# Optimization experiments

Measured on AMD Instinct MI355X. Metric: run time of the kernel, lower is better.

## Reference

```python
import jax, jax.numpy as jnp
import numpy as np

EMBED_DIM = 1024
NUM_HEADS = 16
HEAD_DIM = EMBED_DIM // NUM_HEADS
SCALING = HEAD_DIM ** -0.5
W_SCALE = 0.02  # small init so exp(scores) in focused path stays finite


def setup_inputs() -> dict:
    key = jax.random.key(0)
    ks = jax.random.split(key, 12)
    B, T = 2, 2048
    hidden_states = jax.random.normal(ks[0], (B, T, EMBED_DIM), dtype=jnp.float32)
    focused_attention = jax.random.uniform(ks[1], (B, T, T), dtype=jnp.float32)
    def lin(kw, kb):
        W = jax.random.normal(kw, (EMBED_DIM, EMBED_DIM), dtype=jnp.float32) * W_SCALE
        b = jax.random.normal(kb, (EMBED_DIM,), dtype=jnp.float32) * W_SCALE
        return W, b
    Wq, bq = lin(ks[2], ks[3])
    Wk, bk = lin(ks[4], ks[5])
    Wv, bv = lin(ks[6], ks[7])
    Wo, bo = lin(ks[8], ks[9])
    return {"hidden_states": hidden_states, "focused_attention": focused_attention,
            "Wq": Wq, "bq": bq, "Wk": Wk, "bk": bk, "Wv": Wv, "bv": bv, "Wo": Wo, "bo": bo}


def reference(hidden_states, focused_attention, Wq, bq, Wk, bk, Wv, bv, Wo, bo):
    B, T, D = hidden_states.shape
    H, hd = NUM_HEADS, HEAD_DIM

    def shape_heads(x):  # [B,T,D] -> [B,H,T,hd]
        return x.reshape(B, T, H, hd).transpose(0, 2, 1, 3)

    q = shape_heads((hidden_states @ Wq.T + bq) * SCALING)
    k = shape_heads(hidden_states @ Wk.T + bk)
    v = shape_heads(hidden_states @ Wv.T + bv)

    # [B,H,T,S] raw attention logits
    scores = jnp.einsum('bhtd,bhsd->bhts', q, k)

    # focused_attention path: exp-weighted normalization (not a plain softmax)
    f = focused_attention[:, None, :, :]  # broadcast over heads
    e = f * jnp.exp(scores)
    attn = e / jnp.sum(e, axis=-1, keepdims=True)

    out = jnp.einsum('bhts,bhsd->bhtd', attn, v)  # [B,H,T,hd]
    out = out.transpose(0, 2, 1, 3).reshape(B, T, D)
    return out @ Wo.T + bo
```

## Files before the change

### kernel.cpp

```cpp
#include <hip/hip_runtime.h>
#include <stdint.h>


typedef __attribute__((ext_vector_type(8))) short short8;
typedef __attribute__((ext_vector_type(4))) short short4v;
typedef __attribute__((ext_vector_type(4))) float f32x4;
typedef unsigned short u16;

#define T_SEQ 2048
#define NH    16
#define HD    64
#define DM    1024

__device__ __forceinline__ float b2f(u16 h) {
  union { unsigned u; float f; } v; v.u = ((unsigned)h) << 16; return v.f;
}
__device__ __forceinline__ u16 f2bf(float x) {
  union { float f; unsigned u; } v; v.f = x;
  unsigned r = v.u + 0x7fffu + ((v.u >> 16) & 1u);
  return (u16)(r >> 16);
}
__device__ __forceinline__ short8 cvt8(const float* p) {
  const f32x4 a = *(const f32x4*)p;
  const f32x4 b = *(const f32x4*)(p + 4);
  short8 o;
  o[0] = (short)f2bf(a[0]); o[1] = (short)f2bf(a[1]);
  o[2] = (short)f2bf(a[2]); o[3] = (short)f2bf(a[3]);
  o[4] = (short)f2bf(b[0]); o[5] = (short)f2bf(b[1]);
  o[6] = (short)f2bf(b[2]); o[7] = (short)f2bf(b[3]);
  return o;
}
__device__ __forceinline__ void gl_lds16(const void* g, void* l) {
  __builtin_amdgcn_global_load_lds(
      (const __attribute__((address_space(1))) void*)g,
      (__attribute__((address_space(3))) void*)l, 16, 0, 0);
}

#define HS_CH 524288u
#define F_CH  1048576u
#define W_CH  131072u
__global__ void cvt_kernel(const float* __restrict__ hs, const float* __restrict__ f,
                           const float* __restrict__ Wq, const float* __restrict__ Wk,
                           const float* __restrict__ Wv, const float* __restrict__ Wo,
                           u16* __restrict__ hsb, u16* __restrict__ fb,
                           u16* __restrict__ Wqb, u16* __restrict__ Wkb,
                           u16* __restrict__ Wvb, u16* __restrict__ Wob) {
  unsigned c = blockIdx.x * 256 + threadIdx.x;
  const float* s; u16* d; unsigned off;
  if (c < HS_CH)                       { s = hs; d = hsb; off = c; }
  else if ((c -= HS_CH) < F_CH)        { s = f;  d = fb;  off = c; }
  else if ((c -= F_CH) < W_CH)         { s = Wq; d = Wqb; off = c; }
  else if ((c -= W_CH) < W_CH)         { s = Wk; d = Wkb; off = c; }
  else if ((c -= W_CH) < W_CH)         { s = Wv; d = Wvb; off = c; }
  else                                 { s = Wo; d = Wob; off = c - W_CH; }
  *(short8*)&d[(size_t)off * 8] = cvt8(&s[(size_t)off * 8]);
}

__global__ __launch_bounds__(256, 4) void qkv_kernel(
    const void* __restrict__ Xv,
    const void* __restrict__ Wqv, const float* __restrict__ bq,
    const void* __restrict__ Wkv, const float* __restrict__ bk,
    const void* __restrict__ Wvv, const float* __restrict__ bv,
    int isf32,
    u16* __restrict__ q, u16* __restrict__ k, u16* __restrict__ v)
{
  const int z = blockIdx.z;
  const void* Wp = (z == 0) ? Wqv : (z == 1) ? Wkv : Wvv;
  const float* bias = (z == 0) ? bq : (z == 1) ? bk : bv;

  __shared__ alignas(16) short lsA[4][128][8];
  __shared__ alignas(16) short lsB[4][128][8];

  const int tid = threadIdx.x;
  const int lane = tid & 63;
  const int wv = tid >> 6;
  const int lq = lane >> 4, li = lane & 15;
  const int wm = wv >> 1, wn = wv & 1;

  const int m0 = blockIdx.y * 128;
  const int n0 = blockIdx.x * 128;

  f32x4 acc[4][4];
#pragma unroll
  for (int i = 0; i < 4; i++)
#pragma unroll
    for (int j = 0; j < 4; j++) acc[i][j] = (f32x4){0.f, 0.f, 0.f, 0.f};

  for (int k0 = 0; k0 < DM; k0 += 32) {
    if (isf32) {
      const float* X32 = (const float*)Xv;
      const float* W32 = (const float*)Wp;
#pragma unroll
      for (int r = 0; r < 2; ++r) {
        const int idx = tid + 256 * r;
        const int row = idx >> 2, slab = idx & 3;
        *(short8*)&lsA[slab][row][0] = cvt8(&X32[(size_t)(m0 + row) * DM + k0 + slab * 8]);
        *(short8*)&lsB[slab][row][0] = cvt8(&W32[(size_t)(n0 + row) * DM + k0 + slab * 8]);
      }
    } else {
      const u16* X16 = (const u16*)Xv;
      const u16* W16 = (const u16*)Wp;
#pragma unroll
      for (int r = 0; r < 2; ++r) {
        const int row = r * 64 + lane;
        gl_lds16(&X16[(size_t)(m0 + row) * DM + k0 + wv * 8], &lsA[wv][row][0]);
        gl_lds16(&W16[(size_t)(n0 + row) * DM + k0 + wv * 8], &lsB[wv][row][0]);
      }
    }
    __syncthreads();
    short8 af[4], bf[4];
#pragma unroll
    for (int mt = 0; mt < 4; ++mt)
      af[mt] = *(const short8*)&lsA[lq][wm * 64 + mt * 16 + li][0];
#pragma unroll
    for (int nt = 0; nt < 4; ++nt)
      bf[nt] = *(const short8*)&lsB[lq][wn * 64 + nt * 16 + li][0];
#pragma unroll
    for (int mt = 0; mt < 4; ++mt)
#pragma unroll
      for (int nt = 0; nt < 4; ++nt)
        acc[mt][nt] = __builtin_amdgcn_mfma_f32_16x16x32_bf16(af[mt], bf[nt], acc[mt][nt], 0, 0, 0);
    __syncthreads();
  }

  float bs[4];
#pragma unroll
  for (int nt = 0; nt < 4; ++nt) bs[nt] = bias[n0 + wn * 64 + nt * 16 + li];
  const float scale = (z == 0) ? 0.125f : 1.0f;

  if (z != 2) {
    u16* dst = (z == 0) ? q : k;
#pragma unroll
    for (int mt = 0; mt < 4; ++mt) {
      const int mbase = m0 + wm * 64 + mt * 16 + lq * 4;
#pragma unroll
      for (int nt = 0; nt < 4; ++nt) {
        const int n = n0 + wn * 64 + nt * 16 + li;
        const int h = n >> 6, d = n & 63;
#pragma unroll
        for (int r = 0; r < 4; ++r) {
          const int m = mbase + r;
          const int b = m >> 11, t = m & (T_SEQ - 1);
          dst[((size_t)(b * NH + h) * T_SEQ + t) * HD + d] = f2bf((acc[mt][nt][r] + bs[nt]) * scale);
        }
      }
    }
  } else {
#pragma unroll
    for (int mt = 0; mt < 4; ++mt) {
      const int mbase = m0 + wm * 64 + mt * 16 + lq * 4;
      const int b = mbase >> 11, t = mbase & (T_SEQ - 1);
#pragma unroll
      for (int nt = 0; nt < 4; ++nt) {
        const int n = n0 + wn * 64 + nt * 16 + li;
        const int h = n >> 6, d = n & 63;
        u16 pk[4];
#pragma unroll
        for (int r = 0; r < 4; ++r) pk[r] = f2bf(acc[mt][nt][r] + bs[nt]);
        *(short4v*)&v[((size_t)(b * NH + h) * HD + d) * T_SEQ + t] = *(const short4v*)pk;
      }
    }
  }
}

__global__ __launch_bounds__(256, 2) void attn_kernel(
    const u16* __restrict__ q, const u16* __restrict__ k,
    const u16* __restrict__ v, const void* __restrict__ fv,
    int isf32, u16* __restrict__ ao)
{
  __shared__ alignas(16) u16 Kl[2][8192];
  __shared__ alignas(16) u16 Vl[2][8192];
  __shared__ alignas(16) u16 pPf[4][2048];

  const int tid = threadIdx.x;
  const int w = tid >> 6;
  const int lane = tid & 63;
  const int lq = lane >> 4, li = lane & 15;

  const int t0 = blockIdx.x * 128;
  const int h = blockIdx.y;
  const int b = blockIdx.z;

  const u16* qh = q + (size_t)(b * NH + h) * T_SEQ * HD;
  const u16* kh = k + (size_t)(b * NH + h) * T_SEQ * HD;
  const u16* vh = v + (size_t)(b * NH + h) * HD * T_SEQ;

  short8 qf[2][2];
#pragma unroll
  for (int g = 0; g < 2; ++g)
#pragma unroll
    for (int kk = 0; kk < 2; ++kk)
      qf[g][kk] = *(const short8*)&qh[(size_t)(t0 + w * 32 + g * 16 + li) * HD + kk * 32 + lq * 8];

  f32x4 oacc[2][4];
#pragma unroll
  for (int g = 0; g < 2; ++g)
#pragma unroll
    for (int j = 0; j < 4; j++) oacc[g][j] = (f32x4){0.f, 0.f, 0.f, 0.f};
  float den[2] = {0.f, 0.f};

#define STAGE_TILE(S0, BUF)                                                      \
  {                                                                              \
    const u16* gK = kh + (size_t)(S0) * HD;                                      \
    const u16* gV = vh + (S0);                                                   \
    u16* Kb = &Kl[BUF][0];                                                       \
    u16* Vb = &Vl[BUF][0];                                                       \
    _Pragma("unroll")                                                            \
    for (int r = 0; r < 4; ++r) {                                                \
      const int L = (w * 4 + r) * 64 + lane;                                     \
      const int sl = L >> 3, jx = L & 7, j = jx ^ (sl & 7);                      \
      gl_lds16(gK + (size_t)sl * HD + j * 8, Kb + (size_t)L * 8);                \
      const int d = L >> 4, scx = L & 15, sc = scx ^ (d & 15);                   \
      gl_lds16(gV + (size_t)d * T_SEQ + sc * 8, Vb + (size_t)L * 8);             \
    }                                                                            \
  }

  STAGE_TILE(0, 0)
  __syncthreads();

  for (int it = 0; it < 16; ++it) {
    const int cur = it & 1;
    const int s0 = it * 128;
    if (it < 15) STAGE_TILE(s0 + 128, cur ^ 1)

    const u16* Kb = &Kl[cur][0];
    const u16* Vb = &Vl[cur][0];

    short8 kf[2][8];
#pragma unroll
    for (int kk = 0; kk < 2; ++kk)
#pragma unroll
      for (int mt = 0; mt < 8; ++mt) {
        const int sl = mt * 16 + li;
        const int c = sl * 8 + ((kk * 4 + lq) ^ (sl & 7));
        kf[kk][mt] = *(const short8*)&Kb[(size_t)c * 8];
      }
    short8 vf[4][4];
#pragma unroll
    for (int kk = 0; kk < 4; ++kk)
#pragma unroll
      for (int dn = 0; dn < 4; ++dn) {
        const int d = dn * 16 + li;
        const int c = d * 16 + ((kk * 4 + lq) ^ (d & 15));
        vf[kk][dn] = *(const short8*)&Vb[(size_t)c * 8];
      }

    u16* pw = &pPf[w][0];
#pragma unroll
    for (int g = 0; g < 2; ++g) {
      f32x4 sacc[8];
#pragma unroll
      for (int mt = 0; mt < 8; ++mt) sacc[mt] = (f32x4){0.f, 0.f, 0.f, 0.f};
#pragma unroll
      for (int kk = 0; kk < 2; ++kk)
#pragma unroll
        for (int mt = 0; mt < 8; ++mt)
          sacc[mt] = __builtin_amdgcn_mfma_f32_16x16x32_bf16(kf[kk][mt], qf[g][kk], sacc[mt], 0, 0, 0);

      const int tg = t0 + w * 32 + g * 16 + li;
#pragma unroll
      for (int mt = 0; mt < 8; ++mt) {
        u16 pk[4];
        if (isf32) {
          const float* fb = (const float*)fv + (size_t)b * T_SEQ * T_SEQ;
          const f32x4 fr = *(const f32x4*)&fb[(size_t)tg * T_SEQ + s0 + mt * 16 + lq * 4];
#pragma unroll
          for (int r = 0; r < 4; ++r) {
            const float e = __expf(fminf(sacc[mt][r], 60.0f));
            const float p = fr[r] * e;
            den[g] += p;
            pk[r] = f2bf(p);
          }
        } else {
          const u16* fb = (const u16*)fv + (size_t)b * T_SEQ * T_SEQ;
          const short4v fr = *(const short4v*)&fb[(size_t)tg * T_SEQ + s0 + mt * 16 + lq * 4];
#pragma unroll
          for (int r = 0; r < 4; ++r) {
            const float e = __expf(fminf(sacc[mt][r], 60.0f));
            const float p = b2f((u16)fr[r]) * e;
            den[g] += p;
            pk[r] = f2bf(p);
          }
        }
        const int c8 = (mt * 4 + lq) ^ ((li & 7) << 1);
        *(short4v*)&pw[li * 128 + c8 * 4] = *(const short4v*)pk;
      }

#pragma unroll
      for (int kk = 0; kk < 4; ++kk) {
        const int c8 = ((kk << 3) + (lq << 1)) ^ ((li & 7) << 1);
        const short8 pf = *(const short8*)&pw[li * 128 + c8 * 4];
#pragma unroll
        for (int dn = 0; dn < 4; ++dn)
          oacc[g][dn] = __builtin_amdgcn_mfma_f32_16x16x32_bf16(pf, vf[kk][dn], oacc[g][dn], 0, 0, 0);
      }
    }
    __syncthreads();
  }

#pragma unroll
  for (int g = 0; g < 2; ++g) {
    den[g] += __shfl_xor(den[g], 16, 64);
    den[g] += __shfl_xor(den[g], 32, 64);
  }

#pragma unroll
  for (int g = 0; g < 2; ++g) {
#pragma unroll
    for (int r = 0; r < 4; ++r) {
      const float rd = 1.0f / __shfl(den[g], lq * 4 + r, 64);
      const int t = t0 + w * 32 + g * 16 + lq * 4 + r;
#pragma unroll
      for (int dn = 0; dn < 4; ++dn)
        ao[(size_t)(b * T_SEQ + t) * DM + h * HD + dn * 16 + li] = f2bf(oacc[g][dn][r] * rd);
    }
  }
#undef STAGE_TILE
}

__global__ __launch_bounds__(256, 4) void oproj_kernel(
    const u16* __restrict__ A, const void* __restrict__ Wov,
    const float* __restrict__ bo, int isf32, float* __restrict__ out)
{
  __shared__ alignas(16) short lsA[4][128][8];
  __shared__ alignas(16) short lsB[4][128][8];

  const int tid = threadIdx.x;
  const int lane = tid & 63;
  const int wv = tid >> 6;
  const int lq = lane >> 4, li = lane & 15;
  const int wm = wv >> 1, wn = wv & 1;

  const int m0 = blockIdx.y * 128;
  const int n0 = blockIdx.x * 128;

  f32x4 acc[4][4];
#pragma unroll
  for (int i = 0; i < 4; i++)
#pragma unroll
    for (int j = 0; j < 4; j++) acc[i][j] = (f32x4){0.f, 0.f, 0.f, 0.f};

  for (int k0 = 0; k0 < DM; k0 += 32) {
#pragma unroll
    for (int r = 0; r < 2; ++r) {
      const int row = r * 64 + lane;
      gl_lds16(&A[(size_t)(m0 + row) * DM + k0 + wv * 8], &lsA[wv][row][0]);
    }
    if (isf32) {
      const float* W32 = (const float*)Wov;
#pragma unroll
      for (int r = 0; r < 2; ++r) {
        const int idx = tid + 256 * r;
        const int row = idx >> 2, slab = idx & 3;
        *(short8*)&lsB[slab][row][0] = cvt8(&W32[(size_t)(n0 + row) * DM + k0 + slab * 8]);
      }
    } else {
      const u16* W16 = (const u16*)Wov;
#pragma unroll
      for (int r = 0; r < 2; ++r) {
        const int row = r * 64 + lane;
        gl_lds16(&W16[(size_t)(n0 + row) * DM + k0 + wv * 8], &lsB[wv][row][0]);
      }
    }
    __syncthreads();
    short8 af[4], bf[4];
#pragma unroll
    for (int mt = 0; mt < 4; ++mt)
      af[mt] = *(const short8*)&lsA[lq][wm * 64 + mt * 16 + li][0];
#pragma unroll
    for (int nt = 0; nt < 4; ++nt)
      bf[nt] = *(const short8*)&lsB[lq][wn * 64 + nt * 16 + li][0];
#pragma unroll
    for (int mt = 0; mt < 4; ++mt)
#pragma unroll
      for (int nt = 0; nt < 4; ++nt)
        acc[mt][nt] = __builtin_amdgcn_mfma_f32_16x16x32_bf16(af[mt], bf[nt], acc[mt][nt], 0, 0, 0);
    __syncthreads();
  }

  float bs[4];
#pragma unroll
  for (int nt = 0; nt < 4; ++nt) bs[nt] = bo[n0 + wn * 64 + nt * 16 + li];

#pragma unroll
  for (int mt = 0; mt < 4; ++mt) {
    const int mbase = m0 + wm * 64 + mt * 16 + lq * 4;
#pragma unroll
    for (int nt = 0; nt < 4; ++nt) {
      const int n = n0 + wn * 64 + nt * 16 + li;
#pragma unroll
      for (int r = 0; r < 4; ++r)
        out[(size_t)(mbase + r) * DM + n] = acc[mt][nt][r] + bs[nt];
    }
  }
}

extern "C" void kernel_launch(void* const* d_in, const int* in_sizes, int n_in,
                              void* d_out, int out_size, void* d_ws, size_t ws_size,
                              hipStream_t stream) {
  (void)in_sizes; (void)n_in; (void)out_size;
  const float* hs = (const float*)d_in[0];
  const float* fa = (const float*)d_in[1];
  const float* Wq = (const float*)d_in[2];
  const float* bq = (const float*)d_in[3];
  const float* Wk = (const float*)d_in[4];
  const float* bk = (const float*)d_in[5];
  const float* Wv = (const float*)d_in[6];
  const float* bv = (const float*)d_in[7];
  const float* Wo = (const float*)d_in[8];
  const float* bo = (const float*)d_in[9];
  float* out = (float*)d_out;

  const size_t NEED = 256 + 2u * (8388608u + 4194304u + 4u * 1048576u + 4u * 4194304u);
  char* base = (char*)d_ws + 256;
  if (ws_size >= NEED) {
    u16* fb  = (u16*)base;
    u16* hsb = fb + 8388608u;
    u16* Wqb = hsb + 4194304u;
    u16* Wkb = Wqb + 1048576u;
    u16* Wvb = Wkb + 1048576u;
    u16* Wob = Wvb + 1048576u;
    u16* qw  = Wob + 1048576u;
    u16* kw  = qw + 4194304u;
    u16* vw  = kw + 4194304u;
    u16* aw  = vw + 4194304u;
    cvt_kernel<<<8192, 256, 0, stream>>>(hs, fa, Wq, Wk, Wv, Wo, hsb, fb, Wqb, Wkb, Wvb, Wob);
    qkv_kernel<<<dim3(8, 32, 3), 256, 0, stream>>>(hsb, Wqb, bq, Wkb, bk, Wvb, bv, 0, qw, kw, vw);
    attn_kernel<<<dim3(16, 16, 2), 256, 0, stream>>>(qw, kw, vw, fb, 0, aw);
    oproj_kernel<<<dim3(8, 32, 1), 256, 0, stream>>>(aw, Wob, bo, 0, out);
  } else {
    u16* qw = (u16*)base;
    u16* kw = qw + 4194304u;
    u16* vw = kw + 4194304u;
    u16* aw = vw + 4194304u;
    qkv_kernel<<<dim3(8, 32, 3), 256, 0, stream>>>(hs, Wq, bq, Wk, bk, Wv, bv, 1, qw, kw, vw);
    attn_kernel<<<dim3(16, 16, 2), 256, 0, stream>>>(qw, kw, vw, fa, 1, aw);
    oproj_kernel<<<dim3(8, 32, 1), 256, 0, stream>>>(aw, Wo, bo, 1, out);
  }
}
```

Measured before the change: 341.8 us.

## Prefetch focused-attention tile into registers; store Q/K token-major; stage V transpose via LDS

The attention kernel now loads the next tile's focused_attention values into registers, converted to bf16, while the current tile computes. The loop is unrolled by two to ping-pong between the two register buffers, which hides global-load latency on the largest input stream. Q and K are written in plain [B,T,D] layout with coalesced stores, and the V transpose goes through shared memory so it can use wide 16-byte stores. The cost is more register pressure and the removal of the fminf clamp on the exponent. Rounding f to bf16 in the fp32 path may also change accuracy slightly.

```diff
diff --git a/kernel.cpp b/kernel.cpp
--- a/kernel.cpp
+++ b/kernel.cpp
@@ -68,8 +68,9 @@
   const void* Wp = (z == 0) ? Wqv : (z == 1) ? Wkv : Wvv;
   const float* bias = (z == 0) ? bq : (z == 1) ? bk : bv;
 
-  __shared__ alignas(16) short lsA[4][128][8];
-  __shared__ alignas(16) short lsB[4][128][8];
+  __shared__ alignas(16) u16 smem[17408];
+  u16* lsA = smem;
+  u16* lsB = smem + 4096;
 
   const int tid = threadIdx.x;
   const int lane = tid & 63;
@@ -94,8 +95,8 @@
       for (int r = 0; r < 2; ++r) {
         const int idx = tid + 256 * r;
         const int row = idx >> 2, slab = idx & 3;
-        *(short8*)&lsA[slab][row][0] = cvt8(&X32[(size_t)(m0 + row) * DM + k0 + slab * 8]);
-        *(short8*)&lsB[slab][row][0] = cvt8(&W32[(size_t)(n0 + row) * DM + k0 + slab * 8]);
+        *(short8*)&lsA[(slab * 128 + row) * 8] = cvt8(&X32[(size_t)(m0 + row) * DM + k0 + slab * 8]);
+        *(short8*)&lsB[(slab * 128 + row) * 8] = cvt8(&W32[(size_t)(n0 + row) * DM + k0 + slab * 8]);
       }
     } else {
       const u16* X16 = (const u16*)Xv;
@@ -103,18 +104,18 @@
 #pragma unroll
       for (int r = 0; r < 2; ++r) {
         const int row = r * 64 + lane;
-        gl_lds16(&X16[(size_t)(m0 + row) * DM + k0 + wv * 8], &lsA[wv][row][0]);
-        gl_lds16(&W16[(size_t)(n0 + row) * DM + k0 + wv * 8], &lsB[wv][row][0]);
+        gl_lds16(&X16[(size_t)(m0 + row) * DM + k0 + wv * 8], &lsA[(wv * 128 + row) * 8]);
+        gl_lds16(&W16[(size_t)(n0 + row) * DM + k0 + wv * 8], &lsB[(wv * 128 + row) * 8]);
       }
     }
     __syncthreads();
     short8 af[4], bf[4];
 #pragma unroll
     for (int mt = 0; mt < 4; ++mt)
-      af[mt] = *(const short8*)&lsA[lq][wm * 64 + mt * 16 + li][0];
+      af[mt] = *(const short8*)&lsA[(lq * 128 + wm * 64 + mt * 16 + li) * 8];
 #pragma unroll
     for (int nt = 0; nt < 4; ++nt)
-      bf[nt] = *(const short8*)&lsB[lq][wn * 64 + nt * 16 + li][0];
+      bf[nt] = *(const short8*)&lsB[(lq * 128 + wn * 64 + nt * 16 + li) * 8];
 #pragma unroll
     for (int mt = 0; mt < 4; ++mt)
 #pragma unroll
@@ -126,9 +127,9 @@
   float bs[4];
 #pragma unroll
   for (int nt = 0; nt < 4; ++nt) bs[nt] = bias[n0 + wn * 64 + nt * 16 + li];
-  const float scale = (z == 0) ? 0.125f : 1.0f;
 
   if (z != 2) {
+    const float scale = (z == 0) ? 0.125f : 1.0f;
     u16* dst = (z == 0) ? q : k;
 #pragma unroll
     for (int mt = 0; mt < 4; ++mt) {
@@ -136,29 +137,35 @@
 #pragma unroll
       for (int nt = 0; nt < 4; ++nt) {
         const int n = n0 + wn * 64 + nt * 16 + li;
-        const int h = n >> 6, d = n & 63;
-#pragma unroll
-        for (int r = 0; r < 4; ++r) {
-          const int m = mbase + r;
-          const int b = m >> 11, t = m & (T_SEQ - 1);
-          dst[((size_t)(b * NH + h) * T_SEQ + t) * HD + d] = f2bf((acc[mt][nt][r] + bs[nt]) * scale);
-        }
+#pragma unroll
+        for (int r = 0; r < 4; ++r)
+          dst[(size_t)(mbase + r) * DM + n] = f2bf((acc[mt][nt][r] + bs[nt]) * scale);
       }
     }
   } else {
 #pragma unroll
     for (int mt = 0; mt < 4; ++mt) {
-      const int mbase = m0 + wm * 64 + mt * 16 + lq * 4;
-      const int b = mbase >> 11, t = mbase & (T_SEQ - 1);
+      const int mcol = wm * 64 + mt * 16 + lq * 4;
 #pragma unroll
       for (int nt = 0; nt < 4; ++nt) {
-        const int n = n0 + wn * 64 + nt * 16 + li;
-        const int h = n >> 6, d = n & 63;
+        const int nrow = wn * 64 + nt * 16 + li;
         u16 pk[4];
 #pragma unroll
         for (int r = 0; r < 4; ++r) pk[r] = f2bf(acc[mt][nt][r] + bs[nt]);
-        *(short4v*)&v[((size_t)(b * NH + h) * HD + d) * T_SEQ + t] = *(const short4v*)pk;
-      }
+        *(short4v*)&smem[nrow * 136 + mcol] = *(const short4v*)pk;
+      }
+    }
+    __syncthreads();
+    const int b = m0 >> 11;
+    const int t0 = m0 & (T_SEQ - 1);
+#pragma unroll
+    for (int p = 0; p < 8; ++p) {
+      const int n = p * 16 + (tid >> 4);
+      const int c = tid & 15;
+      const short8 val = *(const short8*)&smem[n * 136 + c * 8];
+      const int ng = n0 + n;
+      const int h = ng >> 6, d = ng & 63;
+      *(short8*)&v[((size_t)(b * NH + h) * HD + d) * T_SEQ + t0 + c * 8] = val;
     }
   }
 }
@@ -181,8 +188,8 @@
   const int h = blockIdx.y;
   const int b = blockIdx.z;
 
-  const u16* qh = q + (size_t)(b * NH + h) * T_SEQ * HD;
-  const u16* kh = k + (size_t)(b * NH + h) * T_SEQ * HD;
+  const u16* qh = q + (size_t)b * T_SEQ * DM + h * HD;
+  const u16* kh = k + (size_t)b * T_SEQ * DM + h * HD;
   const u16* vh = v + (size_t)(b * NH + h) * HD * T_SEQ;
 
   short8 qf[2][2];
@@ -190,7 +197,7 @@
   for (int g = 0; g < 2; ++g)
 #pragma unroll
     for (int kk = 0; kk < 2; ++kk)
-      qf[g][kk] = *(const short8*)&qh[(size_t)(t0 + w * 32 + g * 16 + li) * HD + kk * 32 + lq * 8];
+      qf[g][kk] = *(const short8*)&qh[(size_t)(t0 + w * 32 + g * 16 + li) * DM + kk * 32 + lq * 8];
 
   f32x4 oacc[2][4];
 #pragma unroll
@@ -199,9 +206,11 @@
     for (int j = 0; j < 4; j++) oacc[g][j] = (f32x4){0.f, 0.f, 0.f, 0.f};
   float den[2] = {0.f, 0.f};
 
+  const int tg0 = t0 + w * 32 + li;
+
 #define STAGE_TILE(S0, BUF)                                                      \
   {                                                                              \
-    const u16* gK = kh + (size_t)(S0) * HD;                                      \
+    const u16* gK = kh + (size_t)(S0) * DM;                                      \
     const u16* gV = vh + (S0);                                                   \
     u16* Kb = &Kl[BUF][0];                                                       \
     u16* Vb = &Vl[BUF][0];                                                       \
@@ -209,93 +218,107 @@
     for (int r = 0; r < 4; ++r) {                                                \
       const int L = (w * 4 + r) * 64 + lane;                                     \
       const int sl = L >> 3, jx = L & 7, j = jx ^ (sl & 7);                      \
-      gl_lds16(gK + (size_t)sl * HD + j * 8, Kb + (size_t)L * 8);                \
+      gl_lds16(gK + (size_t)sl * DM + j * 8, Kb + (size_t)L * 8);                \
       const int d = L >> 4, scx = L & 15, sc = scx ^ (d & 15);                   \
       gl_lds16(gV + (size_t)d * T_SEQ + sc * 8, Vb + (size_t)L * 8);             \
     }                                                                            \
   }
 
+#define LOAD_F(S0, FB)                                                           \
+  if (isf32) {                                                                   \
+    const float* f32p = (const float*)fv + (size_t)b * T_SEQ * T_SEQ;            \
+    _Pragma("unroll")                                                            \
+    for (int g = 0; g < 2; ++g)                                                  \
+      _Pragma("unroll")                                                          \
+      for (int mt = 0; mt < 8; ++mt) {                                           \
+        const f32x4 fr = *(const f32x4*)&f32p[(size_t)(tg0 + g * 16) * T_SEQ + (S0) + mt * 16 + lq * 4]; \
+        short4v pk;                                                              \
+        pk[0] = (short)f2bf(fr[0]); pk[1] = (short)f2bf(fr[1]);                  \
+        pk[2] = (short)f2bf(fr[2]); pk[3] = (short)f2bf(fr[3]);                  \
+        FB[g][mt] = pk;                                                          \
+      }                                                                          \
+  } else {                                                                       \
+    const u16* f16p = (const u16*)fv + (size_t)b * T_SEQ * T_SEQ;                \
+    _Pragma("unroll")                                                            \
+    for (int g = 0; g < 2; ++g)                                                  \
+      _Pragma("unroll")                                                          \
+      for (int mt = 0; mt < 8; ++mt)                                             \
+        FB[g][mt] = *(const short4v*)&f16p[(size_t)(tg0 + g * 16) * T_SEQ + (S0) + mt * 16 + lq * 4]; \
+  }
+
+#define ITER_BODY(IT, FCUR, FNXT)                                                \
+  {                                                                              \
+    const int cur = (IT) & 1;                                                    \
+    const int s0 = (IT) * 128;                                                   \
+    if ((IT) < 15) {                                                             \
+      STAGE_TILE(s0 + 128, cur ^ 1)                                              \
+      LOAD_F(s0 + 128, FNXT)                                                     \
+    }                                                                            \
+    const u16* Kb = &Kl[cur][0];                                                 \
+    const u16* Vb = &Vl[cur][0];                                                 \
+    short8 kf[2][8];                                                             \
+    _Pragma("unroll")                                                            \
+    for (int kk = 0; kk < 2; ++kk)                                               \
+      _Pragma("unroll")                                                          \
+      for (int mt = 0; mt < 8; ++mt) {                                           \
+        const int sl = mt * 16 + li;                                             \
+        const int c = sl * 8 + ((kk * 4 + lq) ^ (sl & 7));                       \
+        kf[kk][mt] = *(const short8*)&Kb[(size_t)c * 8];                         \
+      }                                                                          \
+    short8 vf[4][4];                                                             \
+    _Pragma("unroll")                                                            \
+    for (int kk = 0; kk < 4; ++kk)                                               \
+      _Pragma("unroll")                                                          \
+      for (int dn = 0; dn < 4; ++dn) {                                           \
+        const int d = dn * 16 + li;                                              \
+        const int c = d * 16 + ((kk * 4 + lq) ^ (d & 15));                       \
+        vf[kk][dn] = *(const short8*)&Vb[(size_t)c * 8];                         \
+      }                                                                          \
+    u16* pw = &pPf[w][0];                                                        \
+    _Pragma("unroll")                                                            \
+    for (int g = 0; g < 2; ++g) {                                                \
+      f32x4 sacc[8];                                                             \
+      _Pragma("unroll")                                                          \
+      for (int mt = 0; mt < 8; ++mt) sacc[mt] = (f32x4){0.f, 0.f, 0.f, 0.f};     \
+      _Pragma("unroll")                                                          \
+      for (int kk = 0; kk < 2; ++kk)                                             \
+        _Pragma("unroll")                                                        \
+        for (int mt = 0; mt < 8; ++mt)                                           \
+          sacc[mt] = __builtin_amdgcn_mfma_f32_16x16x32_bf16(kf[kk][mt], qf[g][kk], sacc[mt], 0, 0, 0); \
+      _Pragma("unroll")                                                          \
+      for (int mt = 0; mt < 8; ++mt) {                                           \
+        const short4v fr = FCUR[g][mt];                                          \
+        u16 pk[4];                                                               \
+        _Pragma("unroll")                                                        \
+        for (int r = 0; r < 4; ++r) {                                            \
+          const float e = __expf(sacc[mt][r]);                                   \
+          const float p = b2f((u16)fr[r]) * e;                                   \
+          den[g] += p;                                                           \
+          pk[r] = f2bf(p);                                                       \
+        }                                                                        \
+        const int c8 = (mt * 4 + lq) ^ ((li & 7) << 1);                          \
+        *(short4v*)&pw[li * 128 + c8 * 4] = *(const short4v*)pk;                 \
+      }                                                                          \
+      _Pragma("unroll")                                                          \
+      for (int kk = 0; kk < 4; ++kk) {                                           \
+        const int c8 = ((kk << 3) + (lq << 1)) ^ ((li & 7) << 1);                \
+        const short8 pf = *(const short8*)&pw[li * 128 + c8 * 4];                \
+        _Pragma("unroll")                                                        \
+        for (int dn = 0; dn < 4; ++dn)                                           \
+          oacc[g][dn] = __builtin_amdgcn_mfma_f32_16x16x32_bf16(pf, vf[kk][dn], oacc[g][dn], 0, 0, 0); \
+      }                                                                          \
+    }                                                                            \
+    __syncthreads();                                                             \
+  }
+
+  short4v fA[2][8], fB[2][8];
   STAGE_TILE(0, 0)
+  LOAD_F(0, fA)
   __syncthreads();
 
-  for (int it = 0; it < 16; ++it) {
-    const int cur = it & 1;
-    const int s0 = it * 128;
-    if (it < 15) STAGE_TILE(s0 + 128, cur ^ 1)
-
-    const u16* Kb = &Kl[cur][0];
-    const u16* Vb = &Vl[cur][0];
-
-    short8 kf[2][8];
-#pragma unroll
-    for (int kk = 0; kk < 2; ++kk)
-#pragma unroll
-      for (int mt = 0; mt < 8; ++mt) {
-        const int sl = mt * 16 + li;
-        const int c = sl * 8 + ((kk * 4 + lq) ^ (sl & 7));
-        kf[kk][mt] = *(const short8*)&Kb[(size_t)c * 8];
-      }
-    short8 vf[4][4];
-#pragma unroll
-    for (int kk = 0; kk < 4; ++kk)
-#pragma unroll
-      for (int dn = 0; dn < 4; ++dn) {
-        const int d = dn * 16 + li;
-        const int c = d * 16 + ((kk * 4 + lq) ^ (d & 15));
-        vf[kk][dn] = *(const short8*)&Vb[(size_t)c * 8];
-      }
-
-    u16* pw = &pPf[w][0];
-#pragma unroll
-    for (int g = 0; g < 2; ++g) {
-      f32x4 sacc[8];
-#pragma unroll
-      for (int mt = 0; mt < 8; ++mt) sacc[mt] = (f32x4){0.f, 0.f, 0.f, 0.f};
-#pragma unroll
-      for (int kk = 0; kk < 2; ++kk)
-#pragma unroll
-        for (int mt = 0; mt < 8; ++mt)
-          sacc[mt] = __builtin_amdgcn_mfma_f32_16x16x32_bf16(kf[kk][mt], qf[g][kk], sacc[mt], 0, 0, 0);
-
-      const int tg = t0 + w * 32 + g * 16 + li;
-#pragma unroll
-      for (int mt = 0; mt < 8; ++mt) {
-        u16 pk[4];
-        if (isf32) {
-          const float* fb = (const float*)fv + (size_t)b * T_SEQ * T_SEQ;
-          const f32x4 fr = *(const f32x4*)&fb[(size_t)tg * T_SEQ + s0 + mt * 16 + lq * 4];
-#pragma unroll
-          for (int r = 0; r < 4; ++r) {
-            const float e = __expf(fminf(sacc[mt][r], 60.0f));
-            const float p = fr[r] * e;
-            den[g] += p;
-            pk[r] = f2bf(p);
-          }
-        } else {
-          const u16* fb = (const u16*)fv + (size_t)b * T_SEQ * T_SEQ;
-          const short4v fr = *(const short4v*)&fb[(size_t)tg * T_SEQ + s0 + mt * 16 + lq * 4];
-#pragma unroll
-          for (int r = 0; r < 4; ++r) {
-            const float e = __expf(fminf(sacc[mt][r], 60.0f));
-            const float p = b2f((u16)fr[r]) * e;
-            den[g] += p;
-            pk[r] = f2bf(p);
-          }
-        }
-        const int c8 = (mt * 4 + lq) ^ ((li & 7) << 1);
-        *(short4v*)&pw[li * 128 + c8 * 4] = *(const short4v*)pk;
-      }
-
-#pragma unroll
-      for (int kk = 0; kk < 4; ++kk) {
-        const int c8 = ((kk << 3) + (lq << 1)) ^ ((li & 7) << 1);
-        const short8 pf = *(const short8*)&pw[li * 128 + c8 * 4];
-#pragma unroll
-        for (int dn = 0; dn < 4; ++dn)
-          oacc[g][dn] = __builtin_amdgcn_mfma_f32_16x16x32_bf16(pf, vf[kk][dn], oacc[g][dn], 0, 0, 0);
-      }
-    }
-    __syncthreads();
+  for (int it2 = 0; it2 < 16; it2 += 2) {
+    ITER_BODY(it2,     fA, fB)
+    ITER_BODY(it2 + 1, fB, fA)
   }
 
 #pragma unroll
@@ -315,6 +338,8 @@
         ao[(size_t)(b * T_SEQ + t) * DM + h * HD + dn * 16 + li] = f2bf(oacc[g][dn][r] * rd);
     }
   }
+#undef ITER_BODY
+#undef LOAD_F
 #undef STAGE_TILE
 }
 
```

Measured after the change: 429.9 us. 1.26x slower.
